# Optimization experiments

Measured on AMD Instinct MI355X. Metric: run time of the kernel, lower is better.

Reference implementation:

```python
import jax, jax.numpy as jnp
import numpy as np

ID, IH, IW = 8, 16, 16
HEADS, DIM_HEAD = 8, 32
INP, OUP = 256, 256
B = 4
N = ID * IH * IW  # 2048
INNER = HEADS * DIM_HEAD  # 256
SCALE = DIM_HEAD ** -0.5


def _make_relative_pos():
    # Faithful to the torch ctor: 3D coords, pairwise diffs, linearize, shift to >=0
    z, y, x = np.meshgrid(np.arange(ID), np.arange(IH), np.arange(IW), indexing='ij')
    coords = np.stack([z.ravel(), y.ravel(), x.ravel()], axis=1)  # [N,3]
    rel = coords[:, None, :] - coords[None, :, :]                 # [N,N,3]
    rp = rel[:, :, 0] * (IH * IW) + rel[:, :, 1] * IW + rel[:, :, 2]
    rp = rp - rp.min()
    return jnp.asarray(rp, dtype=jnp.int32)                       # [N,N]


def setup_inputs() -> dict:
    key = jax.random.key(0)
    k1, k2, k3, k4, k5 = jax.random.split(key, 5)
    table_size = ID * IH * IW * 8  # 16384, as in nn.Embedding ctor
    return {
        "x": jax.random.normal(k1, (B, N, INP), dtype=jnp.float32),
        "w_qkv": jax.random.normal(k2, (INP, 3 * INNER), dtype=jnp.float32) * (INP ** -0.5),
        "bias_table": jax.random.normal(k3, (table_size, 1), dtype=jnp.float32),
        "w_out": jax.random.normal(k4, (INNER, OUP), dtype=jnp.float32) * (INNER ** -0.5),
        "b_out": jax.random.normal(k5, (OUP,), dtype=jnp.float32),
        "relative_pos": _make_relative_pos(),
    }


def reference(x, w_qkv, bias_table, w_out, b_out, relative_pos):
    Bb, Nn, C = x.shape
    qkv = x @ w_qkv                                   # [B, N, 3*H*D]
    qkv = qkv.reshape(Bb, Nn, 3, HEADS, DIM_HEAD)
    qkv = jnp.transpose(qkv, (2, 0, 3, 1, 4))         # [3, B, H, N, D]
    q, k, v = qkv[0], qkv[1], qkv[2]
    q = q * SCALE
    attn = jnp.einsum('bhnd,bhmd->bhnm', q, k)        # [B, H, N, N]
    bias = bias_table[relative_pos, 0]                # [N, N], shared across B,H
    attn = attn + bias
    attn = jax.nn.softmax(attn, axis=-1)
    out = jnp.einsum('bhnm,bhmd->bhnd', attn, v)      # [B, H, N, D]
    out = jnp.transpose(out, (0, 2, 1, 3)).reshape(Bb, Nn, INNER)
    return out @ w_out + b_out                        # dropout p=0 -> identity
```

## Files before the change

### kernel.cpp

```cpp
#include <hip/hip_runtime.h>

typedef unsigned short u16;
typedef unsigned int u32;
typedef __attribute__((ext_vector_type(8))) short bf16x8;
typedef __attribute__((ext_vector_type(4))) short bf16x4;
typedef __attribute__((ext_vector_type(4))) float f32x4;

#define MFMA16(a, b, c) __builtin_amdgcn_mfma_f32_16x16x32_bf16(a, b, c, 0, 0, 0)
#define MFMAK16(a, b, c) __builtin_amdgcn_mfma_f32_16x16x16bf16_1k(a, b, c, 0, 0, 0)

__device__ __forceinline__ float hw_exp2(float x) { return __builtin_amdgcn_exp2f(x); }

__device__ __forceinline__ u16 f2bf(float f) {
    union { float f; u32 i; } v; v.f = f;
    u32 x = v.i;
    return (u16)((x + 0x7FFFu + ((x >> 16) & 1u)) >> 16);
}

__global__ __launch_bounds__(256) void k_prep(const float* __restrict__ x,
                                              const float* __restrict__ wqkv,
                                              const float* __restrict__ wout,
                                              const float* __restrict__ btab,
                                              u16* __restrict__ xb,
                                              u16* __restrict__ wqkvT,
                                              u16* __restrict__ woutT,
                                              float* __restrict__ stab) {
    const float QSCALE2 = 0.2550566756538019f;
    const float LOG2E = 1.4426950408889634f;
    int bx = blockIdx.x, tid = threadIdx.x;
    if (bx < 1024) {
        int base = bx * 2048 + tid * 8;
        float4 a = *(const float4*)(x + base);
        float4 b = *(const float4*)(x + base + 4);
        uint4 r;
        r.x = f2bf(a.x) | ((u32)f2bf(a.y) << 16);
        r.y = f2bf(a.z) | ((u32)f2bf(a.w) << 16);
        r.z = f2bf(b.x) | ((u32)f2bf(b.y) << 16);
        r.w = f2bf(b.z) | ((u32)f2bf(b.w) << 16);
        *(uint4*)(xb + base) = r;
    } else if (bx < 1792) {
        int idx = (bx - 1024) * 256 + tid;
        int n = idx >> 8, kk = idx & 255;
        float sc = (n < 256) ? QSCALE2 : 1.0f;
        wqkvT[idx] = f2bf(wqkv[kk * 768 + n] * sc);
    } else if (bx < 2048) {
        int idx = (bx - 1792) * 256 + tid;
        int n = idx >> 8, kk = idx & 255;
        woutT[idx] = f2bf(wout[kk * 256 + n]);
    } else {
        int idx = (bx - 2048) * 256 + tid;
        stab[idx] = btab[idx] * LOG2E;
    }
}

__global__ __launch_bounds__(256) void k_gemm_qkv(const u16* __restrict__ xb,
                                                  const u16* __restrict__ wT,
                                                  u16* __restrict__ qkv) {
    __shared__ __align__(16) u16 slds[8704];
    const int tid = threadIdx.x;
    const int wave = tid >> 6, lane = tid & 63, quad = lane >> 4, ql = lane & 15;
    const int mbase = blockIdx.x * 128 + (wave & 1) * 64;
    const int nbase = blockIdx.y * 64 + (wave >> 1) * 32;
    f32x4 acc[4][2];
#pragma unroll
    for (int i = 0; i < 4; ++i)
#pragma unroll
        for (int j = 0; j < 2; ++j) acc[i][j] = (f32x4){0.f, 0.f, 0.f, 0.f};
#pragma unroll
    for (int ks = 0; ks < 8; ++ks) {
        bf16x8 af[4], bfm[2];
#pragma unroll
        for (int ms = 0; ms < 4; ++ms)
            af[ms] = *(const bf16x8*)(xb + (size_t)(mbase + ms * 16 + ql) * 256 + ks * 32 + quad * 8);
#pragma unroll
        for (int ns = 0; ns < 2; ++ns)
            bfm[ns] = *(const bf16x8*)(wT + (size_t)(nbase + ns * 16 + ql) * 256 + ks * 32 + quad * 8);
#pragma unroll
        for (int ms = 0; ms < 4; ++ms)
#pragma unroll
            for (int ns = 0; ns < 2; ++ns)
                acc[ms][ns] = MFMA16(af[ms], bfm[ns], acc[ms][ns]);
    }

    const int t = (blockIdx.y * 64) >> 8;
    if (t < 2) {
        const int rowb = (wave & 1) * 64, colb = (wave >> 1) * 32;
#pragma unroll
        for (int ms = 0; ms < 4; ++ms)
#pragma unroll
            for (int ns = 0; ns < 2; ++ns)
#pragma unroll
                for (int r = 0; r < 4; ++r)
                    slds[(rowb + ms * 16 + quad * 4 + r) * 68 + colb + ns * 16 + ql] =
                        f2bf(acc[ms][ns][r]);
        __syncthreads();
        u16* base = qkv + (size_t)t * 2097152;
#pragma unroll
        for (int p = 0; p < 8; ++p) {
            int c = p * 256 + tid;
            int row = c >> 4, ch = c & 15;
            uint2 w = *(const uint2*)&slds[row * 68 + ch * 4];
            int n = blockIdx.x * 128 + row;
            int col = blockIdx.y * 64 + ch * 4;
            int h = (col & 255) >> 5, d = col & 31;
            *(uint2*)(base + ((size_t)((n >> 11) * 8 + h) * 2048 + (n & 2047)) * 32 + d) = w;
        }
    } else {
        const int hl = wave >> 1, nb = (wave & 1) * 64;
#pragma unroll
        for (int ms = 0; ms < 4; ++ms)
#pragma unroll
            for (int ns = 0; ns < 2; ++ns) {
                u16 e0 = f2bf(acc[ms][ns][0]), e1 = f2bf(acc[ms][ns][1]);
                u16 e2 = f2bf(acc[ms][ns][2]), e3 = f2bf(acc[ms][ns][3]);
                uint2 pp; pp.x = e0 | ((u32)e1 << 16); pp.y = e2 | ((u32)e3 << 16);
                *(uint2*)&slds[(hl * 32 + ns * 16 + ql) * 136 + nb + ms * 16 + quad * 4] = pp;
            }
        __syncthreads();
        u16* vbase = qkv + (size_t)2 * 2097152;
#pragma unroll
        for (int p = 0; p < 4; ++p) {
            int c = p * 256 + tid;
            int row = c >> 4, ch = c & 15;
            bf16x8 w = *(const bf16x8*)&slds[row * 136 + ch * 8];
            int n0 = blockIdx.x * 128 + ch * 8;
            int h = (blockIdx.y & 3) * 2 + (row >> 5), d = row & 31;
            *(bf16x8*)(vbase + (size_t)((n0 >> 11) * 8 + h) * 65536 +
                       (size_t)d * 2048 + (n0 & 2047)) = w;
        }
    }
}

__global__ __launch_bounds__(256, 2) void k_attn(const u16* __restrict__ q,
                                                 const u16* __restrict__ k,
                                                 const u16* __restrict__ vT,
                                                 const float* __restrict__ stab,
                                                 u16* __restrict__ att) {
    __shared__ __align__(16) u16 kbuf[2][2][2048];
    __shared__ __align__(16) u16 vbuf[2][2][2048];
    const int tid = threadIdx.x;
    const int bh = blockIdx.x & 31, qt = blockIdx.x >> 5;
    const int wave = tid >> 6, lane = tid & 63, quad = lane >> 4, ql = lane & 15;

    const u16* kbh = k + (size_t)bh * 65536;
    const u16* vbh = vT + (size_t)bh * 65536;

    const int krow = wave * 16 + (lane >> 2);
    const u16* kg = kbh + krow * 32 + ((((lane & 3) ^ ((lane >> 3) & 3))) << 3);
    const int vd = wave * 8 + (lane >> 3);
    const u16* vg = vbh + (size_t)vd * 2048 + (((lane & 7) ^ (vd & 7)) << 3);

#define GLDS(SRC, DST) __builtin_amdgcn_global_load_lds(                         \
        (const __attribute__((address_space(1))) void*)(SRC),                    \
        (__attribute__((address_space(3))) void*)(DST), 16, 0, 0)
#define DMA(BUF, PAIR) do {                                                      \
    GLDS(kg + (PAIR) * 4096,        &kbuf[BUF][0][wave * 512]);                  \
    GLDS(kg + (PAIR) * 4096 + 2048, &kbuf[BUF][1][wave * 512]);                  \
    GLDS(vg + (PAIR) * 128,         &vbuf[BUF][0][wave * 512]);                  \
    GLDS(vg + (PAIR) * 128 + 64,    &vbuf[BUF][1][wave * 512]);                  \
} while (0)

    DMA(0, 0);

    const float* gtab = stab + qt * 128;

    const int qr0 = qt * 128 + wave * 32 + ql;
    bf16x8 qf[2];
    qf[0] = *(const bf16x8*)(q + ((size_t)bh * 2048 + qr0) * 32 + quad * 8);
    qf[1] = *(const bf16x8*)(q + ((size_t)bh * 2048 + qr0 + 16) * 32 + quad * 8);
    const int bloc0 = wave * 32 + ql + 2047 - quad * 4;
    const int kro = ((quad ^ ((ql >> 1) & 3)) << 3);

    bf16x4 ones4;
#pragma unroll
    for (int i = 0; i < 4; ++i) ones4[i] = (short)0x3F80;

    f32x4 oT0[2], oT1[2], oL[2];
#pragma unroll
    for (int qh = 0; qh < 2; ++qh) {
        oT0[qh] = (f32x4){0.f, 0.f, 0.f, 0.f};
        oT1[qh] = (f32x4){0.f, 0.f, 0.f, 0.f};
        oL[qh]  = (f32x4){0.f, 0.f, 0.f, 0.f};
    }

    __syncthreads();

    for (int pr = 0; pr < 16; ++pr) {
        const int buf = pr & 1;

        f32x4 bc[2][5];
#pragma unroll
        for (int t = 0; t < 2; ++t) {
            const int bkt = bloc0 - (pr * 2 + t) * 64;
#pragma unroll
            for (int g = 0; g < 5; ++g) {
                const float* p = gtab + (bkt + 16 * g - 51);
                bc[t][g] = (f32x4){p[3], p[2], p[1], p[0]};
            }
        }
        __builtin_amdgcn_sched_barrier(0);

        if (pr < 15) DMA(buf ^ 1, pr + 1);

#pragma unroll
        for (int t = 0; t < 2; ++t) {
            const u16* kb = &kbuf[buf][t][0];
            const u16* vb = &vbuf[buf][t][0];
            bf16x8 kf[4];
            bf16x4 va[2][4];
#pragma unroll
            for (int j = 0; j < 4; ++j)
                kf[j] = *(const bf16x8*)(kb + (j * 16 + ql) * 32 + kro);
#pragma unroll
            for (int dt = 0; dt < 2; ++dt)
#pragma unroll
                for (int j = 0; j < 4; ++j) {
                    int nloc = j * 16 + quad * 4;
                    int slot = (nloc >> 3) ^ (ql & 7);
                    va[dt][j] = *(const bf16x4*)(vb + (dt * 16 + ql) * 64 +
                                                 slot * 8 + (nloc & 7));
                }

#pragma unroll
            for (int qh = 0; qh < 2; ++qh) {
                f32x4 s[4];
#pragma unroll
                for (int j = 0; j < 4; ++j)
                    s[j] = MFMA16(kf[j], qf[qh], bc[t][qh + 3 - j]);
#pragma unroll
                for (int j = 0; j < 4; ++j)
#pragma unroll
                    for (int r = 0; r < 4; ++r)
                        s[j][r] = hw_exp2(s[j][r]);
#pragma unroll
                for (int j = 0; j < 4; ++j) {
                    union { u32 u[2]; bf16x4 v; } pj;
                    pj.u[0] = __builtin_amdgcn_perm(__float_as_uint(s[j][1]),
                                                    __float_as_uint(s[j][0]), 0x07060302u);
                    pj.u[1] = __builtin_amdgcn_perm(__float_as_uint(s[j][3]),
                                                    __float_as_uint(s[j][2]), 0x07060302u);
                    oT0[qh] = MFMAK16(va[0][j], pj.v, oT0[qh]);
                    oT1[qh] = MFMAK16(va[1][j], pj.v, oT1[qh]);
                    oL[qh]  = MFMAK16(ones4, pj.v, oL[qh]);
                }
            }
        }
        __syncthreads();
    }
#undef DMA
#undef GLDS

#pragma unroll
    for (int qh = 0; qh < 2; ++qh) {
        float inv = 1.0f / oL[qh][0];
        size_t base = ((size_t)bh * 2048 + qr0 + qh * 16) * 32;
#pragma unroll
        for (int dt = 0; dt < 2; ++dt) {
            const f32x4& o = dt ? oT1[qh] : oT0[qh];
            u16 e0 = f2bf(o[0] * inv), e1 = f2bf(o[1] * inv);
            u16 e2 = f2bf(o[2] * inv), e3 = f2bf(o[3] * inv);
            uint2 pp; pp.x = e0 | ((u32)e1 << 16); pp.y = e2 | ((u32)e3 << 16);
            *(uint2*)(att + base + dt * 16 + quad * 4) = pp;
        }
    }
}

__global__ __launch_bounds__(256) void k_gemm_out(const u16* __restrict__ attq,
                                                  const u16* __restrict__ wT,
                                                  const float* __restrict__ bout,
                                                  float* __restrict__ out) {
    const int tid = threadIdx.x;
    const int wave = tid >> 6, lane = tid & 63, quad = lane >> 4, ql = lane & 15;
    const int mbase = blockIdx.x * 128 + (wave & 1) * 64;
    const int nbase = blockIdx.y * 64 + (wave >> 1) * 32;
    f32x4 acc[4][2];
#pragma unroll
    for (int i = 0; i < 4; ++i)
#pragma unroll
        for (int j = 0; j < 2; ++j) acc[i][j] = (f32x4){0.f, 0.f, 0.f, 0.f};
#pragma unroll
    for (int ks = 0; ks < 8; ++ks) {
        bf16x8 af[4], bfm[2];
#pragma unroll
        for (int ms = 0; ms < 4; ++ms) {
            int row = mbase + ms * 16 + ql;
            af[ms] = *(const bf16x8*)(attq +
                ((size_t)((row >> 11) * 8 + ks) * 2048 + (row & 2047)) * 32 + quad * 8);
        }
#pragma unroll
        for (int ns = 0; ns < 2; ++ns)
            bfm[ns] = *(const bf16x8*)(wT + (size_t)(nbase + ns * 16 + ql) * 256 + ks * 32 + quad * 8);
#pragma unroll
        for (int ms = 0; ms < 4; ++ms)
#pragma unroll
            for (int ns = 0; ns < 2; ++ns)
                acc[ms][ns] = MFMA16(af[ms], bfm[ns], acc[ms][ns]);
    }
#pragma unroll
    for (int ms = 0; ms < 4; ++ms)
#pragma unroll
        for (int ns = 0; ns < 2; ++ns)
#pragma unroll
            for (int r = 0; r < 4; ++r) {
                int Mrow = mbase + ms * 16 + quad * 4 + r;
                int col = nbase + ns * 16 + ql;
                out[(size_t)Mrow * 256 + col] = acc[ms][ns][r] + bout[col];
            }
}

extern "C" void kernel_launch(void* const* d_in, const int* in_sizes, int n_in,
                              void* d_out, int out_size, void* d_ws, size_t ws_size,
                              hipStream_t stream) {
    const float* x    = (const float*)d_in[0];
    const float* wqkv = (const float*)d_in[1];
    const float* btab = (const float*)d_in[2];
    const float* wout = (const float*)d_in[3];
    const float* bout = (const float*)d_in[4];
    float* out = (float*)d_out;

    if (ws_size < (size_t)13172736) return;
    u16* ws = (u16*)d_ws;
    u16* wqkvT = ws;
    u16* woutT = wqkvT + 196608;
    u16* qkv   = woutT + 65536;
    float* stab = (float*)(qkv + 6291456);
    u16* xb    = (u16*)d_out;

    hipLaunchKernelGGL(k_prep, dim3(2112), dim3(256), 0, stream, x, wqkv, wout, btab,
                       xb, wqkvT, woutT, stab);
    hipLaunchKernelGGL(k_gemm_qkv, dim3(64, 12), dim3(256), 0, stream, xb, wqkvT, qkv);
    hipLaunchKernelGGL(k_attn, dim3(512), dim3(256), 0, stream,
                       qkv, qkv + 2097152, qkv + 2 * 2097152, stab, qkv);
    hipLaunchKernelGGL(k_gemm_out, dim3(64, 4), dim3(256), 0, stream, qkv, woutT, bout, out);
}
```

Before: 141.1 us.

## Fuse all stages into one persistent kernel with software grid barriers

Merges the prep, QKV GEMM, attention and output GEMM kernels into a single 512-block persistent kernel separated by atomic-counter grid barriers, with a memset resetting the counters each call. This removes inter-kernel launch gaps and tail drain between stages. The output GEMM is retiled to 32-column tiles so all 512 blocks get work. It relies on all blocks being co-resident to avoid deadlock and adds spin-barrier overhead plus uneven work in the QKV phase.

```diff
diff --git a/kernel.cpp b/kernel.cpp
--- a/kernel.cpp
+++ b/kernel.cpp
@@ -17,295 +17,303 @@
     return (u16)((x + 0x7FFFu + ((x >> 16) & 1u)) >> 16);
 }
 
-__global__ __launch_bounds__(256) void k_prep(const float* __restrict__ x,
-                                              const float* __restrict__ wqkv,
-                                              const float* __restrict__ wout,
-                                              const float* __restrict__ btab,
-                                              u16* __restrict__ xb,
-                                              u16* __restrict__ wqkvT,
-                                              u16* __restrict__ woutT,
-                                              float* __restrict__ stab) {
-    const float QSCALE2 = 0.2550566756538019f;
-    const float LOG2E = 1.4426950408889634f;
-    int bx = blockIdx.x, tid = threadIdx.x;
-    if (bx < 1024) {
-        int base = bx * 2048 + tid * 8;
-        float4 a = *(const float4*)(x + base);
-        float4 b = *(const float4*)(x + base + 4);
-        uint4 r;
-        r.x = f2bf(a.x) | ((u32)f2bf(a.y) << 16);
-        r.y = f2bf(a.z) | ((u32)f2bf(a.w) << 16);
-        r.z = f2bf(b.x) | ((u32)f2bf(b.y) << 16);
-        r.w = f2bf(b.z) | ((u32)f2bf(b.w) << 16);
-        *(uint4*)(xb + base) = r;
-    } else if (bx < 1792) {
-        int idx = (bx - 1024) * 256 + tid;
-        int n = idx >> 8, kk = idx & 255;
-        float sc = (n < 256) ? QSCALE2 : 1.0f;
-        wqkvT[idx] = f2bf(wqkv[kk * 768 + n] * sc);
-    } else if (bx < 2048) {
-        int idx = (bx - 1792) * 256 + tid;
-        int n = idx >> 8, kk = idx & 255;
-        woutT[idx] = f2bf(wout[kk * 256 + n]);
-    } else {
-        int idx = (bx - 2048) * 256 + tid;
-        stab[idx] = btab[idx] * LOG2E;
-    }
+__device__ __forceinline__ void grid_barrier(u32* bar, int slot) {
+    __syncthreads();
+    if (threadIdx.x == 0) {
+        __threadfence();
+        atomicAdd(&bar[slot], 1u);
+        while (atomicAdd(&bar[slot], 0u) < 512u) __builtin_amdgcn_s_sleep(2);
+        __threadfence();
+    }
+    __syncthreads();
 }
 
-__global__ __launch_bounds__(256) void k_gemm_qkv(const u16* __restrict__ xb,
-                                                  const u16* __restrict__ wT,
-                                                  u16* __restrict__ qkv) {
-    __shared__ __align__(16) u16 slds[8704];
-    const int tid = threadIdx.x;
+__global__ __launch_bounds__(256, 2) void k_fused(
+    const float* __restrict__ x, const float* __restrict__ wqkv,
+    const float* __restrict__ btab, const float* __restrict__ wout,
+    const float* __restrict__ bout, float* __restrict__ out,
+    u16* __restrict__ wqkvT, u16* __restrict__ woutT,
+    u16* __restrict__ qkv, float* __restrict__ stab,
+    u16* __restrict__ xb, u32* __restrict__ bar) {
+
+    __shared__ __align__(16) u16 smem[16384];
+    const int bid = blockIdx.x, tid = threadIdx.x;
     const int wave = tid >> 6, lane = tid & 63, quad = lane >> 4, ql = lane & 15;
-    const int mbase = blockIdx.x * 128 + (wave & 1) * 64;
-    const int nbase = blockIdx.y * 64 + (wave >> 1) * 32;
-    f32x4 acc[4][2];
-#pragma unroll
-    for (int i = 0; i < 4; ++i)
-#pragma unroll
-        for (int j = 0; j < 2; ++j) acc[i][j] = (f32x4){0.f, 0.f, 0.f, 0.f};
-#pragma unroll
-    for (int ks = 0; ks < 8; ++ks) {
-        bf16x8 af[4], bfm[2];
-#pragma unroll
-        for (int ms = 0; ms < 4; ++ms)
-            af[ms] = *(const bf16x8*)(xb + (size_t)(mbase + ms * 16 + ql) * 256 + ks * 32 + quad * 8);
-#pragma unroll
-        for (int ns = 0; ns < 2; ++ns)
-            bfm[ns] = *(const bf16x8*)(wT + (size_t)(nbase + ns * 16 + ql) * 256 + ks * 32 + quad * 8);
-#pragma unroll
-        for (int ms = 0; ms < 4; ++ms)
+
+    {
+        const float QSCALE2 = 0.2550566756538019f;
+        const float LOG2E = 1.4426950408889634f;
+        for (int u = bid; u < 2112; u += 512) {
+            if (u < 1024) {
+                int base = u * 2048 + tid * 8;
+                float4 a = *(const float4*)(x + base);
+                float4 b = *(const float4*)(x + base + 4);
+                uint4 r;
+                r.x = f2bf(a.x) | ((u32)f2bf(a.y) << 16);
+                r.y = f2bf(a.z) | ((u32)f2bf(a.w) << 16);
+                r.z = f2bf(b.x) | ((u32)f2bf(b.y) << 16);
+                r.w = f2bf(b.z) | ((u32)f2bf(b.w) << 16);
+                *(uint4*)(xb + base) = r;
+            } else if (u < 1792) {
+                int idx = (u - 1024) * 256 + tid;
+                int n = idx >> 8, kk = idx & 255;
+                float sc = (n < 256) ? QSCALE2 : 1.0f;
+                wqkvT[idx] = f2bf(wqkv[kk * 768 + n] * sc);
+            } else if (u < 2048) {
+                int idx = (u - 1792) * 256 + tid;
+                int n = idx >> 8, kk = idx & 255;
+                woutT[idx] = f2bf(wout[kk * 256 + n]);
+            } else {
+                int idx = (u - 2048) * 256 + tid;
+                stab[idx] = btab[idx] * LOG2E;
+            }
+        }
+    }
+    grid_barrier(bar, 0);
+
+    for (int u = bid; u < 768; u += 512) {
+        const int bx = u & 63, by = u >> 6;
+        u16* slds = smem;
+        const int mbase = bx * 128 + (wave & 1) * 64;
+        const int nbase = by * 64 + (wave >> 1) * 32;
+        f32x4 acc[4][2];
+#pragma unroll
+        for (int i = 0; i < 4; ++i)
+#pragma unroll
+            for (int j = 0; j < 2; ++j) acc[i][j] = (f32x4){0.f, 0.f, 0.f, 0.f};
+#pragma unroll
+        for (int ks = 0; ks < 8; ++ks) {
+            bf16x8 af[4], bfm[2];
+#pragma unroll
+            for (int ms = 0; ms < 4; ++ms)
+                af[ms] = *(const bf16x8*)(xb + (size_t)(mbase + ms * 16 + ql) * 256 + ks * 32 + quad * 8);
 #pragma unroll
             for (int ns = 0; ns < 2; ++ns)
-                acc[ms][ns] = MFMA16(af[ms], bfm[ns], acc[ms][ns]);
-    }
-
-    const int t = (blockIdx.y * 64) >> 8;
-    if (t < 2) {
-        const int rowb = (wave & 1) * 64, colb = (wave >> 1) * 32;
-#pragma unroll
-        for (int ms = 0; ms < 4; ++ms)
-#pragma unroll
-            for (int ns = 0; ns < 2; ++ns)
-#pragma unroll
-                for (int r = 0; r < 4; ++r)
-                    slds[(rowb + ms * 16 + quad * 4 + r) * 68 + colb + ns * 16 + ql] =
-                        f2bf(acc[ms][ns][r]);
+                bfm[ns] = *(const bf16x8*)(wqkvT + (size_t)(nbase + ns * 16 + ql) * 256 + ks * 32 + quad * 8);
+#pragma unroll
+            for (int ms = 0; ms < 4; ++ms)
+#pragma unroll
+                for (int ns = 0; ns < 2; ++ns)
+                    acc[ms][ns] = MFMA16(af[ms], bfm[ns], acc[ms][ns]);
+        }
+
+        const int t = (by * 64) >> 8;
+        if (t < 2) {
+            const int rowb = (wave & 1) * 64, colb = (wave >> 1) * 32;
+#pragma unroll
+            for (int ms = 0; ms < 4; ++ms)
+#pragma unroll
+                for (int ns = 0; ns < 2; ++ns)
+#pragma unroll
+                    for (int r = 0; r < 4; ++r)
+                        slds[(rowb + ms * 16 + quad * 4 + r) * 68 + colb + ns * 16 + ql] =
+                            f2bf(acc[ms][ns][r]);
+            __syncthreads();
+            u16* base = qkv + (size_t)t * 2097152;
+#pragma unroll
+            for (int p = 0; p < 8; ++p) {
+                int c = p * 256 + tid;
+                int row = c >> 4, ch = c & 15;
+                uint2 w = *(const uint2*)&slds[row * 68 + ch * 4];
+                int n = bx * 128 + row;
+                int col = by * 64 + ch * 4;
+                int h = (col & 255) >> 5, d = col & 31;
+                *(uint2*)(base + ((size_t)((n >> 11) * 8 + h) * 2048 + (n & 2047)) * 32 + d) = w;
+            }
+        } else {
+            const int hl = wave >> 1, nb = (wave & 1) * 64;
+#pragma unroll
+            for (int ms = 0; ms < 4; ++ms)
+#pragma unroll
+                for (int ns = 0; ns < 2; ++ns) {
+                    u16 e0 = f2bf(acc[ms][ns][0]), e1 = f2bf(acc[ms][ns][1]);
+                    u16 e2 = f2bf(acc[ms][ns][2]), e3 = f2bf(acc[ms][ns][3]);
+                    uint2 pp; pp.x = e0 | ((u32)e1 << 16); pp.y = e2 | ((u32)e3 << 16);
+                    *(uint2*)&slds[(hl * 32 + ns * 16 + ql) * 136 + nb + ms * 16 + quad * 4] = pp;
+                }
+            __syncthreads();
+            u16* vbase = qkv + (size_t)2 * 2097152;
+#pragma unroll
+            for (int p = 0; p < 4; ++p) {
+                int c = p * 256 + tid;
+                int row = c >> 4, ch = c & 15;
+                bf16x8 w = *(const bf16x8*)&slds[row * 136 + ch * 8];
+                int n0 = bx * 128 + ch * 8;
+                int h = (by & 3) * 2 + (row >> 5), d = row & 31;
+                *(bf16x8*)(vbase + (size_t)((n0 >> 11) * 8 + h) * 65536 +
+                           (size_t)d * 2048 + (n0 & 2047)) = w;
+            }
+        }
         __syncthreads();
-        u16* base = qkv + (size_t)t * 2097152;
-#pragma unroll
-        for (int p = 0; p < 8; ++p) {
-            int c = p * 256 + tid;
-            int row = c >> 4, ch = c & 15;
-            uint2 w = *(const uint2*)&slds[row * 68 + ch * 4];
-            int n = blockIdx.x * 128 + row;
-            int col = blockIdx.y * 64 + ch * 4;
-            int h = (col & 255) >> 5, d = col & 31;
-            *(uint2*)(base + ((size_t)((n >> 11) * 8 + h) * 2048 + (n & 2047)) * 32 + d) = w;
-        }
-    } else {
-        const int hl = wave >> 1, nb = (wave & 1) * 64;
-#pragma unroll
-        for (int ms = 0; ms < 4; ++ms)
-#pragma unroll
-            for (int ns = 0; ns < 2; ++ns) {
-                u16 e0 = f2bf(acc[ms][ns][0]), e1 = f2bf(acc[ms][ns][1]);
-                u16 e2 = f2bf(acc[ms][ns][2]), e3 = f2bf(acc[ms][ns][3]);
-                uint2 pp; pp.x = e0 | ((u32)e1 << 16); pp.y = e2 | ((u32)e3 << 16);
-                *(uint2*)&slds[(hl * 32 + ns * 16 + ql) * 136 + nb + ms * 16 + quad * 4] = pp;
-            }
-        __syncthreads();
-        u16* vbase = qkv + (size_t)2 * 2097152;
-#pragma unroll
-        for (int p = 0; p < 4; ++p) {
-            int c = p * 256 + tid;
-            int row = c >> 4, ch = c & 15;
-            bf16x8 w = *(const bf16x8*)&slds[row * 136 + ch * 8];
-            int n0 = blockIdx.x * 128 + ch * 8;
-            int h = (blockIdx.y & 3) * 2 + (row >> 5), d = row & 31;
-            *(bf16x8*)(vbase + (size_t)((n0 >> 11) * 8 + h) * 65536 +
-                       (size_t)d * 2048 + (n0 & 2047)) = w;
-        }
-    }
-}
-
-__global__ __launch_bounds__(256, 2) void k_attn(const u16* __restrict__ q,
-                                                 const u16* __restrict__ k,
-                                                 const u16* __restrict__ vT,
-                                                 const float* __restrict__ stab,
-                                                 u16* __restrict__ att) {
-    __shared__ __align__(16) u16 kbuf[2][2][2048];
-    __shared__ __align__(16) u16 vbuf[2][2][2048];
-    const int tid = threadIdx.x;
-    const int bh = blockIdx.x & 31, qt = blockIdx.x >> 5;
-    const int wave = tid >> 6, lane = tid & 63, quad = lane >> 4, ql = lane & 15;
-
-    const u16* kbh = k + (size_t)bh * 65536;
-    const u16* vbh = vT + (size_t)bh * 65536;
-
-    const int krow = wave * 16 + (lane >> 2);
-    const u16* kg = kbh + krow * 32 + ((((lane & 3) ^ ((lane >> 3) & 3))) << 3);
-    const int vd = wave * 8 + (lane >> 3);
-    const u16* vg = vbh + (size_t)vd * 2048 + (((lane & 7) ^ (vd & 7)) << 3);
+    }
+    grid_barrier(bar, 1);
+
+    {
+        const u16* q = qkv;
+        const u16* k = qkv + 2097152;
+        const u16* vT = qkv + 2 * 2097152;
+        u16* att = qkv;
+        const int bh = bid & 31, qt = bid >> 5;
+
+#define KB(BUF, T) (smem + (BUF) * 4096 + (T) * 2048)
+#define VB(BUF, T) (smem + 8192 + (BUF) * 4096 + (T) * 2048)
+
+        const u16* kbh = k + (size_t)bh * 65536;
+        const u16* vbh = vT + (size_t)bh * 65536;
+
+        const int krow = wave * 16 + (lane >> 2);
+        const u16* kg = kbh + krow * 32 + ((((lane & 3) ^ ((lane >> 3) & 3))) << 3);
+        const int vd = wave * 8 + (lane >> 3);
+        const u16* vg = vbh + (size_t)vd * 2048 + (((lane & 7) ^ (vd & 7)) << 3);
 
 #define GLDS(SRC, DST) __builtin_amdgcn_global_load_lds(                         \
         (const __attribute__((address_space(1))) void*)(SRC),                    \
         (__attribute__((address_space(3))) void*)(DST), 16, 0, 0)
 #define DMA(BUF, PAIR) do {                                                      \
-    GLDS(kg + (PAIR) * 4096,        &kbuf[BUF][0][wave * 512]);                  \
-    GLDS(kg + (PAIR) * 4096 + 2048, &kbuf[BUF][1][wave * 512]);                  \
-    GLDS(vg + (PAIR) * 128,         &vbuf[BUF][0][wave * 512]);                  \
-    GLDS(vg + (PAIR) * 128 + 64,    &vbuf[BUF][1][wave * 512]);                  \
+    GLDS(kg + (PAIR) * 4096,        KB(BUF, 0) + wave * 512);                    \
+    GLDS(kg + (PAIR) * 4096 + 2048, KB(BUF, 1) + wave * 512);                    \
+    GLDS(vg + (PAIR) * 128,         VB(BUF, 0) + wave * 512);                    \
+    GLDS(vg + (PAIR) * 128 + 64,    VB(BUF, 1) + wave * 512);                    \
 } while (0)
 
-    DMA(0, 0);
-
-    const float* gtab = stab + qt * 128;
-
-    const int qr0 = qt * 128 + wave * 32 + ql;
-    bf16x8 qf[2];
-    qf[0] = *(const bf16x8*)(q + ((size_t)bh * 2048 + qr0) * 32 + quad * 8);
-    qf[1] = *(const bf16x8*)(q + ((size_t)bh * 2048 + qr0 + 16) * 32 + quad * 8);
-    const int bloc0 = wave * 32 + ql + 2047 - quad * 4;
-    const int kro = ((quad ^ ((ql >> 1) & 3)) << 3);
-
-    bf16x4 ones4;
-#pragma unroll
-    for (int i = 0; i < 4; ++i) ones4[i] = (short)0x3F80;
-
-    f32x4 oT0[2], oT1[2], oL[2];
-#pragma unroll
-    for (int qh = 0; qh < 2; ++qh) {
-        oT0[qh] = (f32x4){0.f, 0.f, 0.f, 0.f};
-        oT1[qh] = (f32x4){0.f, 0.f, 0.f, 0.f};
-        oL[qh]  = (f32x4){0.f, 0.f, 0.f, 0.f};
-    }
-
-    __syncthreads();
-
-    for (int pr = 0; pr < 16; ++pr) {
-        const int buf = pr & 1;
-
-        f32x4 bc[2][5];
-#pragma unroll
-        for (int t = 0; t < 2; ++t) {
-            const int bkt = bloc0 - (pr * 2 + t) * 64;
-#pragma unroll
-            for (int g = 0; g < 5; ++g) {
-                const float* p = gtab + (bkt + 16 * g - 51);
-                bc[t][g] = (f32x4){p[3], p[2], p[1], p[0]};
-            }
-        }
-        __builtin_amdgcn_sched_barrier(0);
-
-        if (pr < 15) DMA(buf ^ 1, pr + 1);
-
-#pragma unroll
-        for (int t = 0; t < 2; ++t) {
-            const u16* kb = &kbuf[buf][t][0];
-            const u16* vb = &vbuf[buf][t][0];
-            bf16x8 kf[4];
-            bf16x4 va[2][4];
-#pragma unroll
-            for (int j = 0; j < 4; ++j)
-                kf[j] = *(const bf16x8*)(kb + (j * 16 + ql) * 32 + kro);
-#pragma unroll
-            for (int dt = 0; dt < 2; ++dt)
-#pragma unroll
-                for (int j = 0; j < 4; ++j) {
-                    int nloc = j * 16 + quad * 4;
-                    int slot = (nloc >> 3) ^ (ql & 7);
-                    va[dt][j] = *(const bf16x4*)(vb + (dt * 16 + ql) * 64 +
-                                                 slot * 8 + (nloc & 7));
+        DMA(0, 0);
+
+        const float* gtab = stab + qt * 128;
+
+        const int qr0 = qt * 128 + wave * 32 + ql;
+        bf16x8 qf[2];
+        qf[0] = *(const bf16x8*)(q + ((size_t)bh * 2048 + qr0) * 32 + quad * 8);
+        qf[1] = *(const bf16x8*)(q + ((size_t)bh * 2048 + qr0 + 16) * 32 + quad * 8);
+        const int bloc0 = wave * 32 + ql + 2047 - quad * 4;
+        const int kro = ((quad ^ ((ql >> 1) & 3)) << 3);
+
+        bf16x4 ones4;
+#pragma unroll
+        for (int i = 0; i < 4; ++i) ones4[i] = (short)0x3F80;
+
+        f32x4 oT0[2], oT1[2], oL[2];
+#pragma unroll
+        for (int qh = 0; qh < 2; ++qh) {
+            oT0[qh] = (f32x4){0.f, 0.f, 0.f, 0.f};
+            oT1[qh] = (f32x4){0.f, 0.f, 0.f, 0.f};
+            oL[qh]  = (f32x4){0.f, 0.f, 0.f, 0.f};
+        }
+
+        __syncthreads();
+
+        for (int pr = 0; pr < 16; ++pr) {
+            const int buf = pr & 1;
+
+            f32x4 bc[2][5];
+#pragma unroll
+            for (int t = 0; t < 2; ++t) {
+                const int bkt = bloc0 - (pr * 2 + t) * 64;
+#pragma unroll
+                for (int g = 0; g < 5; ++g) {
+                    const float* p = gtab + (bkt + 16 * g - 51);
+                    bc[t][g] = (f32x4){p[3], p[2], p[1], p[0]};
                 }
-
-#pragma unroll
-            for (int qh = 0; qh < 2; ++qh) {
-                f32x4 s[4];
+            }
+            __builtin_amdgcn_sched_barrier(0);
+
+            if (pr < 15) DMA(buf ^ 1, pr + 1);
+
+#pragma unroll
+            for (int t = 0; t < 2; ++t) {
+                const u16* kb = KB(buf, t);
+                const u16* vb = VB(buf, t);
+                bf16x8 kf[4];
+                bf16x4 va[2][4];
 #pragma unroll
                 for (int j = 0; j < 4; ++j)
-                    s[j] = MFMA16(kf[j], qf[qh], bc[t][qh + 3 - j]);
-#pragma unroll
-                for (int j = 0; j < 4; ++j)
-#pragma unroll
-                    for (int r = 0; r < 4; ++r)
-                        s[j][r] = hw_exp2(s[j][r]);
-#pragma unroll
-                for (int j = 0; j < 4; ++j) {
-                    union { u32 u[2]; bf16x4 v; } pj;
-                    pj.u[0] = __builtin_amdgcn_perm(__float_as_uint(s[j][1]),
-                                                    __float_as_uint(s[j][0]), 0x07060302u);
-                    pj.u[1] = __builtin_amdgcn_perm(__float_as_uint(s[j][3]),
-                                                    __float_as_uint(s[j][2]), 0x07060302u);
-                    oT0[qh] = MFMAK16(va[0][j], pj.v, oT0[qh]);
-                    oT1[qh] = MFMAK16(va[1][j], pj.v, oT1[qh]);
-                    oL[qh]  = MFMAK16(ones4, pj.v, oL[qh]);
+                    kf[j] = *(const bf16x8*)(kb + (j * 16 + ql) * 32 + kro);
+#pragma unroll
+                for (int dt = 0; dt < 2; ++dt)
+#pragma unroll
+                    for (int j = 0; j < 4; ++j) {
+                        int nloc = j * 16 + quad * 4;
+                        int slot = (nloc >> 3) ^ (ql & 7);
+                        va[dt][j] = *(const bf16x4*)(vb + (dt * 16 + ql) * 64 +
+                                                     slot * 8 + (nloc & 7));
+                    }
+
+#pragma unroll
+                for (int qh = 0; qh < 2; ++qh) {
+                    f32x4 s[4];
+#pragma unroll
+                    for (int j = 0; j < 4; ++j)
+                        s[j] = MFMA16(kf[j], qf[qh], bc[t][qh + 3 - j]);
+#pragma unroll
+                    for (int j = 0; j < 4; ++j)
+#pragma unroll
+                        for (int r = 0; r < 4; ++r)
+                            s[j][r] = hw_exp2(s[j][r]);
+#pragma unroll
+                    for (int j = 0; j < 4; ++j) {
+                        union { u32 u[2]; bf16x4 v; } pj;
+                        pj.u[0] = __builtin_amdgcn_perm(__float_as_uint(s[j][1]),
+                                                        __float_as_uint(s[j][0]), 0x07060302u);
+                        pj.u[1] = __builtin_amdgcn_perm(__float_as_uint(s[j][3]),
+                                                        __float_as_uint(s[j][2]), 0x07060302u);
+                        oT0[qh] = MFMAK16(va[0][j], pj.v, oT0[qh]);
+                        oT1[qh] = MFMAK16(va[1][j], pj.v, oT1[qh]);
+                        oL[qh]  = MFMAK16(ones4, pj.v, oL[qh]);
+                    }
                 }
             }
-        }
-        __syncthreads();
-    }
+            __syncthreads();
+        }
 #undef DMA
 #undef GLDS
-
-#pragma unroll
-    for (int qh = 0; qh < 2; ++qh) {
-        float inv = 1.0f / oL[qh][0];
-        size_t base = ((size_t)bh * 2048 + qr0 + qh * 16) * 32;
-#pragma unroll
-        for (int dt = 0; dt < 2; ++dt) {
-            const f32x4& o = dt ? oT1[qh] : oT0[qh];
-            u16 e0 = f2bf(o[0] * inv), e1 = f2bf(o[1] * inv);
-            u16 e2 = f2bf(o[2] * inv), e3 = f2bf(o[3] * inv);
-            uint2 pp; pp.x = e0 | ((u32)e1 << 16); pp.y = e2 | ((u32)e3 << 16);
-            *(uint2*)(att + base + dt * 16 + quad * 4) = pp;
-        }
-    }
-}
-
-__global__ __launch_bounds__(256) void k_gemm_out(const u16* __restrict__ attq,
-                                                  const u16* __restrict__ wT,
-                                                  const float* __restrict__ bout,
-                                                  float* __restrict__ out) {
-    const int tid = threadIdx.x;
-    const int wave = tid >> 6, lane = tid & 63, quad = lane >> 4, ql = lane & 15;
-    const int mbase = blockIdx.x * 128 + (wave & 1) * 64;
-    const int nbase = blockIdx.y * 64 + (wave >> 1) * 32;
-    f32x4 acc[4][2];
-#pragma unroll
-    for (int i = 0; i < 4; ++i)
-#pragma unroll
-        for (int j = 0; j < 2; ++j) acc[i][j] = (f32x4){0.f, 0.f, 0.f, 0.f};
-#pragma unroll
-    for (int ks = 0; ks < 8; ++ks) {
-        bf16x8 af[4], bfm[2];
-#pragma unroll
-        for (int ms = 0; ms < 4; ++ms) {
-            int row = mbase + ms * 16 + ql;
-            af[ms] = *(const bf16x8*)(attq +
-                ((size_t)((row >> 11) * 8 + ks) * 2048 + (row & 2047)) * 32 + quad * 8);
-        }
-#pragma unroll
-        for (int ns = 0; ns < 2; ++ns)
-            bfm[ns] = *(const bf16x8*)(wT + (size_t)(nbase + ns * 16 + ql) * 256 + ks * 32 + quad * 8);
+#undef KB
+#undef VB
+
+#pragma unroll
+        for (int qh = 0; qh < 2; ++qh) {
+            float inv = 1.0f / oL[qh][0];
+            size_t base = ((size_t)bh * 2048 + qr0 + qh * 16) * 32;
+#pragma unroll
+            for (int dt = 0; dt < 2; ++dt) {
+                const f32x4& o = dt ? oT1[qh] : oT0[qh];
+                u16 e0 = f2bf(o[0] * inv), e1 = f2bf(o[1] * inv);
+                u16 e2 = f2bf(o[2] * inv), e3 = f2bf(o[3] * inv);
+                uint2 pp; pp.x = e0 | ((u32)e1 << 16); pp.y = e2 | ((u32)e3 << 16);
+                *(uint2*)(att + base + dt * 16 + quad * 4) = pp;
+            }
+        }
+    }
+    grid_barrier(bar, 2);
+
+    {
+        const int bx = bid & 63, by = bid >> 6;
+        const int mbase = bx * 128 + (wave & 1) * 64;
+        const int nb = by * 32 + (wave >> 1) * 16;
+        f32x4 acc[4];
+#pragma unroll
+        for (int i = 0; i < 4; ++i) acc[i] = (f32x4){0.f, 0.f, 0.f, 0.f};
+#pragma unroll
+        for (int ks = 0; ks < 8; ++ks) {
+            bf16x8 af[4], bfm;
+#pragma unroll
+            for (int ms = 0; ms < 4; ++ms) {
+                int row = mbase + ms * 16 + ql;
+                af[ms] = *(const bf16x8*)(qkv +
+                    ((size_t)((row >> 11) * 8 + ks) * 2048 + (row & 2047)) * 32 + quad * 8);
+            }
+            bfm = *(const bf16x8*)(woutT + (size_t)(nb + ql) * 256 + ks * 32 + quad * 8);
+#pragma unroll
+            for (int ms = 0; ms < 4; ++ms)
+                acc[ms] = MFMA16(af[ms], bfm, acc[ms]);
+        }
+        const float bo = bout[nb + ql];
 #pragma unroll
         for (int ms = 0; ms < 4; ++ms)
-#pragma unroll
-            for (int ns = 0; ns < 2; ++ns)
-                acc[ms][ns] = MFMA16(af[ms], bfm[ns], acc[ms][ns]);
-    }
-#pragma unroll
-    for (int ms = 0; ms < 4; ++ms)
-#pragma unroll
-        for (int ns = 0; ns < 2; ++ns)
 #pragma unroll
             for (int r = 0; r < 4; ++r) {
                 int Mrow = mbase + ms * 16 + quad * 4 + r;
-                int col = nbase + ns * 16 + ql;
-                out[(size_t)Mrow * 256 + col] = acc[ms][ns][r] + bout[col];
-            }
+                out[(size_t)Mrow * 256 + (nb + ql)] = acc[ms][r] + bo;
+            }
+    }
 }
 
 extern "C" void kernel_launch(void* const* d_in, const int* in_sizes, int n_in,
@@ -318,18 +326,17 @@
     const float* bout = (const float*)d_in[4];
     float* out = (float*)d_out;
 
-    if (ws_size < (size_t)13172736) return;
+    if (ws_size < (size_t)13172800) return;
     u16* ws = (u16*)d_ws;
     u16* wqkvT = ws;
     u16* woutT = wqkvT + 196608;
     u16* qkv   = woutT + 65536;
     float* stab = (float*)(qkv + 6291456);
+    u32* bar   = (u32*)((char*)d_ws + 13172736);
     u16* xb    = (u16*)d_out;
 
-    hipLaunchKernelGGL(k_prep, dim3(2112), dim3(256), 0, stream, x, wqkv, wout, btab,
-                       xb, wqkvT, woutT, stab);
-    hipLaunchKernelGGL(k_gemm_qkv, dim3(64, 12), dim3(256), 0, stream, xb, wqkvT, qkv);
-    hipLaunchKernelGGL(k_attn, dim3(512), dim3(256), 0, stream,
-                       qkv, qkv + 2097152, qkv + 2 * 2097152, stab, qkv);
-    hipLaunchKernelGGL(k_gemm_out, dim3(64, 4), dim3(256), 0, stream, qkv, woutT, bout, out);
+    hipMemsetAsync(bar, 0, 64, stream);
+    hipLaunchKernelGGL(k_fused, dim3(512), dim3(256), 0, stream,
+                       x, wqkv, btab, wout, bout, out,
+                       wqkvT, woutT, qkv, stab, xb, bar);
 }
```

Measured after the change: 289.2 us. +105.0%, slower.
